# Optimization experiments

Hardware: AMD Instinct MI355X
Metric: run time of the kernel (lower is better)

Reference implementation:

```python
import jax, jax.numpy as jnp
import numpy as np


def setup_inputs() -> dict:
    key = jax.random.key(0)
    B, D, C, H = 4096, 64, 128, 512
    ks = jax.random.split(key, 6)
    return {
        "q_z_x_params": jax.random.normal(ks[0], (B, C), jnp.float32),
        "eps": jax.random.normal(ks[1], (B, D), jnp.float32),
        "W1": jax.random.normal(ks[2], (D + C, H), jnp.float32) / np.sqrt(D + C).astype(np.float32),
        "b1": jnp.zeros((H,), jnp.float32),
        "W2": jax.random.normal(ks[3], (H, H), jnp.float32) / np.sqrt(H).astype(np.float32),
        "b2": jnp.zeros((H,), jnp.float32),
        "W3": jax.random.normal(ks[4], (H, 2 * D), jnp.float32) / np.sqrt(H).astype(np.float32),
        "b3": jnp.zeros((2 * D,), jnp.float32),
    }


def _made_masks(D, C, H):
    # Standard MADE degrees, natural ordering; context columns fully connected.
    m_in = np.arange(1, D + 1)                      # input degrees 1..D
    m_h = (np.arange(H) % (D - 1)) + 1              # hidden degrees 1..D-1
    M1 = np.concatenate([m_h[None, :] >= m_in[:, None],
                         np.ones((C, H), bool)], axis=0)   # (D+C, H)
    M2 = m_h[None, :] >= m_h[:, None]               # (H, H)
    m_out = np.tile(np.arange(1, D + 1), 2)         # (2D,) mean||prescale
    M3 = m_out[None, :] > m_h[:, None]              # (H, 2D)
    f32 = jnp.float32
    return jnp.asarray(M1, f32), jnp.asarray(M2, f32), jnp.asarray(M3, f32)


def reference(q_z_x_params, eps, W1, b1, W2, b2, W3, b3):
    B, D = eps.shape
    C = q_z_x_params.shape[1]
    H = W2.shape[0]
    M1, M2, M3 = _made_masks(D, C, H)
    mW1, mW2, mW3 = W1 * M1, W2 * M2, W3 * M3

    def made(z):
        x = jnp.concatenate([z, q_z_x_params], axis=1)   # (B, D+C)
        h1 = jax.nn.relu(x @ mW1 + b1)
        h2 = jax.nn.relu(h1 @ mW2 + b2)
        out = h2 @ mW3 + b3                              # (B, 2D)
        return out[:, :D], out[:, D:]

    def step(z, i):
        mean, prescale = made(z)
        mu_i = jnp.take(mean, i, axis=1)                 # (B,)
        scale_i = jax.nn.softplus(jnp.take(prescale, i, axis=1))
        z_i = mu_i + scale_i * jnp.take(eps, i, axis=1)  # reparameterized Normal sample
        z = z.at[:, i].set(z_i)
        return z, None

    z0 = jnp.zeros((B, D), eps.dtype)
    z_sample, _ = jax.lax.scan(step, z0, jnp.arange(D))
    return z_sample
```

## Files before the change

kernel.cpp:

```cpp
#include <hip/hip_runtime.h>
#include <math.h>

#define DD 64
#define CC 128
#define HH 512
#define BATCH 4096

__global__ void transpose_w3(const float* __restrict__ W3, float* __restrict__ W3T) {
    int idx = blockIdx.x * blockDim.x + threadIdx.x;
    int c = idx >> 9;
    int j = idx & 511;
    W3T[idx] = W3[j * (2 * DD) + c];
}

__device__ __forceinline__ void load8s(const float* __restrict__ p, float* r) {
    float4 a = *(const float4*)(p);
    float4 b = *(const float4*)(p + 4);
    r[0] = a.x; r[1] = a.y; r[2] = a.z; r[3] = a.w;
    r[4] = b.x; r[5] = b.y; r[6] = b.z; r[7] = b.w;
}

__device__ __forceinline__ float fast_softplus(float x) {
    float t = exp2f(-fabsf(x) * 1.44269504f);
    return fmaxf(x, 0.f) + 0.69314718f * log2f(1.f + t);
}

__device__ __forceinline__ float bcast(float x, int l) {
    return __int_as_float(__builtin_amdgcn_readlane(__float_as_int(x), l));
}

#define DPP_ADD(x, ctrl, rm)                                                          \
    x += __int_as_float(__builtin_amdgcn_update_dpp(0, __float_as_int(x), ctrl, rm, 0xf, true))
__device__ __forceinline__ float wave_allsum(float x) {
    DPP_ADD(x, 0x111, 0xf);
    DPP_ADD(x, 0x112, 0xf);
    DPP_ADD(x, 0x114, 0xf);
    DPP_ADD(x, 0x118, 0xf);
    DPP_ADD(x, 0x142, 0xa);
    DPP_ADD(x, 0x143, 0xc);
    return bcast(x, 63);
}

typedef const __attribute__((address_space(1))) void* as1_cptr;
typedef __attribute__((address_space(3))) void* as3_ptr;
__device__ __forceinline__ void glds16(const float* g, float* l) {
    __builtin_amdgcn_global_load_lds((as1_cptr)g, (as3_ptr)l, 16, 0, 0);
}

__global__ __launch_bounds__(256, 1) void made_sample(
    const float* __restrict__ ctx,
    const float* __restrict__ eps,
    const float* __restrict__ W1,
    const float* __restrict__ b1,
    const float* __restrict__ W2,
    const float* __restrict__ b2,
    const float* __restrict__ b3,
    const float* __restrict__ W3T,
    float* __restrict__ out)
{
    const int lane  = threadIdx.x & 63;
    const int w     = threadIdx.x >> 6;
    const int rbase = blockIdx.x * 16 + w * 4;
    const int jbase = 8 * lane;

    __shared__ float sbuf[2][12 * HH];

    int deg[8];
    #pragma unroll
    for (int u = 0; u < 8; ++u) deg[u] = (jbase + u) % 63 + 1;

    float p1[4][8], p2[4][8], h2[4][8];
    {
        float t1[8], t2[8];
        load8s(b1 + jbase, t1);
        load8s(b2 + jbase, t2);
        #pragma unroll
        for (int r = 0; r < 4; ++r)
            #pragma unroll
            for (int u = 0; u < 8; ++u) { p1[r][u] = t1[u]; p2[r][u] = t2[u]; h2[r][u] = 0.f; }
    }

    float ca[4], cb[4], ep[4];
    #pragma unroll
    for (int r = 0; r < 4; ++r) {
        ca[r] = ctx[(rbase + r) * CC + lane];
        cb[r] = ctx[(rbase + r) * CC + 64 + lane];
        ep[r] = eps[(rbase + r) * DD + lane];
    }
    const float b3m = b3[lane];
    const float b3p = b3[64 + lane];

    auto stage_ctx = [&](int ch, float* buf) {
        #pragma unroll
        for (int q2 = 0; q2 < 2; ++q2) {
            const int q = 2 * w + q2;
            const float* src = W1 + (DD + 8 * ch + q) * HH;
            glds16(src + lane * 4, buf + q * HH);
            glds16(src + 256 + lane * 4, buf + q * HH + 256);
        }
    };
    auto stage_step = [&](int in, float* buf) {
        const int basen = (in == 0) ? 0 : (in - 1);
        #pragma unroll
        for (int rr = 0; rr < 3; ++rr) {
            const int r = w + 4 * rr;
            const float* src;
            if (r < 9) {
                int k = basen + 63 * r;
                if (k >= HH) k = HH - 8;
                src = W2 + k * HH;
            } else if (r == 9) {
                src = W3T + in * HH;
            } else if (r == 10) {
                src = W3T + (DD + in) * HH;
            } else {
                src = W1 + in * HH;
            }
            glds16(src + lane * 4, buf + r * HH);
            glds16(src + 256 + lane * 4, buf + r * HH + 256);
        }
    };

    stage_ctx(0, sbuf[0]);
    __syncthreads();
    #pragma unroll 1
    for (int ch = 0; ch < 16; ++ch) {
        float* cur = sbuf[ch & 1];
        float* nxt = sbuf[(ch + 1) & 1];
        if (ch < 15) stage_ctx(ch + 1, nxt);
        else         stage_step(0, sbuf[0]);
        #pragma unroll
        for (int q = 0; q < 8; ++q) {
            float wv[8];
            load8s(cur + q * HH + jbase, wv);
            const int c = 8 * ch + q;
            #pragma unroll
            for (int r = 0; r < 4; ++r) {
                const float srcv = (ch < 8) ? ca[r] : cb[r];
                const float cv = bcast(srcv, c & 63);
                #pragma unroll
                for (int u = 0; u < 8; ++u) p1[r][u] = fmaf(cv, wv[u], p1[r][u]);
            }
        }
        __syncthreads();
    }

    float z[4] = {0.f, 0.f, 0.f, 0.f};

    #pragma unroll 1
    for (int i = 0; i < DD; ++i) {
        float* cur = sbuf[i & 1];
        float* nxt = sbuf[(i + 1) & 1];
        if (i < 63) stage_step(i + 1, nxt);

        float wm[8], wp[8], w1r[8];
        load8s(cur + 9 * HH + jbase, wm);
        load8s(cur + 10 * HH + jbase, wp);
        load8s(cur + 11 * HH + jbase, w1r);

        float m[4];
        #pragma unroll
        for (int r = 0; r < 4; ++r) {
            float mv = 0.f;
            #pragma unroll
            for (int u = 0; u < 8; ++u) mv = (deg[u] == i) ? p1[r][u] : mv;
            m[r] = fmaxf(mv, 0.f);
        }

        const int base = (i == 0) ? 0 : (i - 1);
        #pragma unroll
        for (int t = 0; t < 9; ++t) {
            const int k = base + 63 * t;
            float wv[8];
            load8s(cur + t * HH + jbase, wv);
            float ha[4];
            if (t == 8) {
                const float vm = (k < HH) ? 1.f : 0.f;
                #pragma unroll
                for (int r = 0; r < 4; ++r) ha[r] = vm * bcast(m[r], 63);
            } else {
                #pragma unroll
                for (int r = 0; r < 4; ++r) ha[r] = bcast(m[r], k >> 3);
            }
            #pragma unroll
            for (int u = 0; u < 8; ++u)
                #pragma unroll
                for (int r = 0; r < 4; ++r) p2[r][u] = fmaf(ha[r], wv[u], p2[r][u]);
        }

        #pragma unroll
        for (int r = 0; r < 4; ++r)
            #pragma unroll
            for (int u = 0; u < 8; ++u)
                if (deg[u] == i) h2[r][u] = fmaxf(p2[r][u], 0.f);

        float macc[4], qacc[4];
        #pragma unroll
        for (int r = 0; r < 4; ++r) {
            float ma = 0.f, qa = 0.f;
            #pragma unroll
            for (int u = 0; u < 8; ++u) {
                ma = fmaf(h2[r][u], wm[u], ma);
                qa = fmaf(h2[r][u], wp[u], qa);
            }
            macc[r] = ma; qacc[r] = qa;
        }
        const float bm = bcast(b3m, i);
        const float bp = bcast(b3p, i);
        #pragma unroll
        for (int r = 0; r < 4; ++r) {
            const float mt = wave_allsum(macc[r]) + bm;
            const float qt = wave_allsum(qacc[r]) + bp;
            const float sp = fast_softplus(qt);
            const float ei = bcast(ep[r], i);
            const float zi = fmaf(sp, ei, mt);
            if (lane == i) z[r] = zi;
            #pragma unroll
            for (int u = 0; u < 8; ++u) p1[r][u] = fmaf(zi, w1r[u], p1[r][u]);
        }

        __syncthreads();
    }

    #pragma unroll
    for (int r = 0; r < 4; ++r) out[(rbase + r) * DD + lane] = z[r];
}

extern "C" void kernel_launch(void* const* d_in, const int* in_sizes, int n_in,
                              void* d_out, int out_size, void* d_ws, size_t ws_size,
                              hipStream_t stream) {
    const float* ctx = (const float*)d_in[0];
    const float* eps = (const float*)d_in[1];
    const float* W1  = (const float*)d_in[2];
    const float* b1  = (const float*)d_in[3];
    const float* W2  = (const float*)d_in[4];
    const float* b2  = (const float*)d_in[5];
    const float* W3  = (const float*)d_in[6];
    const float* b3  = (const float*)d_in[7];
    float* W3T = (float*)d_ws;

    transpose_w3<<<(2 * DD * HH) / 256, 256, 0, stream>>>(W3, W3T);
    made_sample<<<BATCH / 16, 256, 0, stream>>>(ctx, eps, W1, b1, W2, b2, b3, W3T,
                                                (float*)d_out);
}
```

Before: 202.9 us.

## Halve rows per block for two blocks per CU and permute LDS row layout

Each wave now handles 2 batch rows instead of 4. The grid doubles to 512 blocks, and launch bounds allow two blocks per CU, so the latency-bound 64-step sequential loop has more resident waves to interleave. Weight rows are staged into LDS with a permuted layout so each lane reads two contiguous float4s at lane*4 and 256+lane*4 instead of a strided 8-float chunk, which should reduce LDS bank conflicts. The cost is that every block restages the same weights, so total LDS staging traffic and global weight reads per batch row double.

After: 191.2 us. -5.8%, faster.

```diff
diff --git a/kernel.cpp b/kernel.cpp
--- a/kernel.cpp
+++ b/kernel.cpp
@@ -11,13 +11,6 @@
     int c = idx >> 9;
     int j = idx & 511;
     W3T[idx] = W3[j * (2 * DD) + c];
-}
-
-__device__ __forceinline__ void load8s(const float* __restrict__ p, float* r) {
-    float4 a = *(const float4*)(p);
-    float4 b = *(const float4*)(p + 4);
-    r[0] = a.x; r[1] = a.y; r[2] = a.z; r[3] = a.w;
-    r[4] = b.x; r[5] = b.y; r[6] = b.z; r[7] = b.w;
 }
 
 __device__ __forceinline__ float fast_softplus(float x) {
@@ -47,7 +40,7 @@
     __builtin_amdgcn_global_load_lds((as1_cptr)g, (as3_ptr)l, 16, 0, 0);
 }
 
-__global__ __launch_bounds__(256, 1) void made_sample(
+__global__ __launch_bounds__(256, 2) void made_sample(
     const float* __restrict__ ctx,
     const float* __restrict__ eps,
     const float* __restrict__ W1,
@@ -60,7 +53,7 @@
 {
     const int lane  = threadIdx.x & 63;
     const int w     = threadIdx.x >> 6;
-    const int rbase = blockIdx.x * 16 + w * 4;
+    const int rbase = blockIdx.x * 8 + w * 2;
     const int jbase = 8 * lane;
 
     __shared__ float sbuf[2][12 * HH];
@@ -69,20 +62,32 @@
     #pragma unroll
     for (int u = 0; u < 8; ++u) deg[u] = (jbase + u) % 63 + 1;
 
-    float p1[4][8], p2[4][8], h2[4][8];
+    auto load8lds = [&](const float* base, float* r) {
+        float4 a = *(const float4*)(base + lane * 4);
+        float4 b = *(const float4*)(base + 256 + lane * 4);
+        r[0] = a.x; r[1] = a.y; r[2] = a.z; r[3] = a.w;
+        r[4] = b.x; r[5] = b.y; r[6] = b.z; r[7] = b.w;
+    };
+    auto stage_row = [&](const float* src, float* dst) {
+        glds16(src + lane * 8,     dst);
+        glds16(src + lane * 8 + 4, dst + 256);
+    };
+
+    float p1[2][8], p2[2][8], h2[2][8];
     {
-        float t1[8], t2[8];
-        load8s(b1 + jbase, t1);
-        load8s(b2 + jbase, t2);
-        #pragma unroll
-        for (int r = 0; r < 4; ++r)
-            #pragma unroll
-            for (int u = 0; u < 8; ++u) { p1[r][u] = t1[u]; p2[r][u] = t2[u]; h2[r][u] = 0.f; }
-    }
-
-    float ca[4], cb[4], ep[4];
+        #pragma unroll
+        for (int u = 0; u < 8; ++u) {
+            float t1 = b1[jbase + u];
+            float t2 = b2[jbase + u];
+            p1[0][u] = t1; p1[1][u] = t1;
+            p2[0][u] = t2; p2[1][u] = t2;
+            h2[0][u] = 0.f; h2[1][u] = 0.f;
+        }
+    }
+
+    float ca[2], cb[2], ep[2];
     #pragma unroll
-    for (int r = 0; r < 4; ++r) {
+    for (int r = 0; r < 2; ++r) {
         ca[r] = ctx[(rbase + r) * CC + lane];
         cb[r] = ctx[(rbase + r) * CC + 64 + lane];
         ep[r] = eps[(rbase + r) * DD + lane];
@@ -94,9 +99,7 @@
         #pragma unroll
         for (int q2 = 0; q2 < 2; ++q2) {
             const int q = 2 * w + q2;
-            const float* src = W1 + (DD + 8 * ch + q) * HH;
-            glds16(src + lane * 4, buf + q * HH);
-            glds16(src + 256 + lane * 4, buf + q * HH + 256);
+            stage_row(W1 + (DD + 8 * ch + q) * HH, buf + q * HH);
         }
     };
     auto stage_step = [&](int in, float* buf) {
@@ -116,8 +119,7 @@
             } else {
                 src = W1 + in * HH;
             }
-            glds16(src + lane * 4, buf + r * HH);
-            glds16(src + 256 + lane * 4, buf + r * HH + 256);
+            stage_row(src, buf + r * HH);
         }
     };
 
@@ -132,10 +134,10 @@
         #pragma unroll
         for (int q = 0; q < 8; ++q) {
             float wv[8];
-            load8s(cur + q * HH + jbase, wv);
+            load8lds(cur + q * HH, wv);
             const int c = 8 * ch + q;
             #pragma unroll
-            for (int r = 0; r < 4; ++r) {
+            for (int r = 0; r < 2; ++r) {
                 const float srcv = (ch < 8) ? ca[r] : cb[r];
                 const float cv = bcast(srcv, c & 63);
                 #pragma unroll
@@ -145,7 +147,7 @@
         __syncthreads();
     }
 
-    float z[4] = {0.f, 0.f, 0.f, 0.f};
+    float z[2] = {0.f, 0.f};
 
     #pragma unroll 1
     for (int i = 0; i < DD; ++i) {
@@ -154,13 +156,13 @@
         if (i < 63) stage_step(i + 1, nxt);
 
         float wm[8], wp[8], w1r[8];
-        load8s(cur + 9 * HH + jbase, wm);
-        load8s(cur + 10 * HH + jbase, wp);
-        load8s(cur + 11 * HH + jbase, w1r);
-
-        float m[4];
-        #pragma unroll
-        for (int r = 0; r < 4; ++r) {
+        load8lds(cur + 9 * HH, wm);
+        load8lds(cur + 10 * HH, wp);
+        load8lds(cur + 11 * HH, w1r);
+
+        float m[2];
+        #pragma unroll
+        for (int r = 0; r < 2; ++r) {
             float mv = 0.f;
             #pragma unroll
             for (int u = 0; u < 8; ++u) mv = (deg[u] == i) ? p1[r][u] : mv;
@@ -172,31 +174,31 @@
         for (int t = 0; t < 9; ++t) {
             const int k = base + 63 * t;
             float wv[8];
-            load8s(cur + t * HH + jbase, wv);
-            float ha[4];
+            load8lds(cur + t * HH, wv);
+            float ha[2];
             if (t == 8) {
                 const float vm = (k < HH) ? 1.f : 0.f;
                 #pragma unroll
-                for (int r = 0; r < 4; ++r) ha[r] = vm * bcast(m[r], 63);
+                for (int r = 0; r < 2; ++r) ha[r] = vm * bcast(m[r], 63);
             } else {
                 #pragma unroll
-                for (int r = 0; r < 4; ++r) ha[r] = bcast(m[r], k >> 3);
+                for (int r = 0; r < 2; ++r) ha[r] = bcast(m[r], k >> 3);
             }
             #pragma unroll
             for (int u = 0; u < 8; ++u)
                 #pragma unroll
-                for (int r = 0; r < 4; ++r) p2[r][u] = fmaf(ha[r], wv[u], p2[r][u]);
-        }
-
-        #pragma unroll
-        for (int r = 0; r < 4; ++r)
+                for (int r = 0; r < 2; ++r) p2[r][u] = fmaf(ha[r], wv[u], p2[r][u]);
+        }
+
+        #pragma unroll
+        for (int r = 0; r < 2; ++r)
             #pragma unroll
             for (int u = 0; u < 8; ++u)
                 if (deg[u] == i) h2[r][u] = fmaxf(p2[r][u], 0.f);
 
-        float macc[4], qacc[4];
-        #pragma unroll
-        for (int r = 0; r < 4; ++r) {
+        float macc[2], qacc[2];
+        #pragma unroll
+        for (int r = 0; r < 2; ++r) {
             float ma = 0.f, qa = 0.f;
             #pragma unroll
             for (int u = 0; u < 8; ++u) {
@@ -208,7 +210,7 @@
         const float bm = bcast(b3m, i);
         const float bp = bcast(b3p, i);
         #pragma unroll
-        for (int r = 0; r < 4; ++r) {
+        for (int r = 0; r < 2; ++r) {
             const float mt = wave_allsum(macc[r]) + bm;
             const float qt = wave_allsum(qacc[r]) + bp;
             const float sp = fast_softplus(qt);
@@ -223,7 +225,7 @@
     }
 
     #pragma unroll
-    for (int r = 0; r < 4; ++r) out[(rbase + r) * DD + lane] = z[r];
+    for (int r = 0; r < 2; ++r) out[(rbase + r) * DD + lane] = z[r];
 }
 
 extern "C" void kernel_launch(void* const* d_in, const int* in_sizes, int n_in,
@@ -240,6 +242,6 @@
     float* W3T = (float*)d_ws;
 
     transpose_w3<<<(2 * DD * HH) / 256, 256, 0, stream>>>(W3, W3T);
-    made_sample<<<BATCH / 16, 256, 0, stream>>>(ctx, eps, W1, b1, W2, b2, b3, W3T,
-                                                (float*)d_out);
-}
+    made_sample<<<BATCH / 8, 256, 0, stream>>>(ctx, eps, W1, b1, W2, b2, b3, W3T,
+                                               (float*)d_out);
+}
```
